# Optimization experiments

Measured on AMD Instinct MI355X. Metric: run time of the kernel, lower is better.

Reference implementation:

```python
import jax, jax.numpy as jnp
import numpy as np


def _maxpool2(t):
    # 2x2x2 max pool, stride 2. t: [B, C, D, H, W]
    B, C, D, H, W = t.shape
    return t.reshape(B, C, D // 2, 2, H // 2, 2, W // 2, 2).max(axis=(3, 5, 7))


def setup_inputs() -> dict:
    key = jax.random.key(0)
    ks = jax.random.split(key, 5)
    ch = 64
    B, D, H, W = 2, 32, 32, 32
    x = jax.random.normal(ks[0], (B, ch, D, H, W), dtype=jnp.float32)
    # 1x1x1 conv weights (out_ch, in_ch), Kaiming-ish scale
    w_theta = jax.random.normal(ks[1], (ch // 8, ch), dtype=jnp.float32) / np.sqrt(ch)
    w_phi = jax.random.normal(ks[2], (ch // 8, ch), dtype=jnp.float32) / np.sqrt(ch)
    w_g = jax.random.normal(ks[3], (ch // 2, ch), dtype=jnp.float32) / np.sqrt(ch)
    w_o = jax.random.normal(ks[4], (ch, ch // 2), dtype=jnp.float32) / np.sqrt(ch // 2)
    gamma = jnp.ones((), dtype=jnp.float32)  # original inits at 0; 1 gives nontrivial output
    return {"x": x, "w_theta": w_theta, "w_phi": w_phi, "w_g": w_g, "w_o": w_o, "gamma": gamma}


def reference(x, w_theta, w_phi, w_g, w_o, gamma):
    B, C, D, H, W = x.shape
    N = D * H * W
    M = N // 8
    xf = x.reshape(B, C, N)  # [B, C, N]
    # 1x1x1 convs = channel matmuls
    theta = jnp.einsum('oc,bcn->bon', w_theta, xf)                     # [B, C//8, N]
    phi = _maxpool2(jnp.einsum('oc,bcn->bon', w_phi, xf).reshape(B, C // 8, D, H, W)).reshape(B, C // 8, M)
    g = _maxpool2(jnp.einsum('oc,bcn->bon', w_g, xf).reshape(B, C // 2, D, H, W)).reshape(B, C // 2, M)
    # unscaled attention: softmax over keys (M)
    beta = jax.nn.softmax(jnp.einsum('bcn,bcm->bnm', theta, phi), axis=-1)  # [B, N, M]
    o = jnp.einsum('bcm,bnm->bcn', g, beta)                                 # [B, C//2, N]
    out = gamma * jnp.einsum('oc,bcn->bon', w_o, o).reshape(B, C, D, H, W) + x
    return out
```

## Files before the change

### kernel.cpp

```cpp
#include <hip/hip_runtime.h>
#include <cstdint>
#include <cstddef>

typedef __attribute__((ext_vector_type(4))) short short4v;
typedef __attribute__((ext_vector_type(4))) float float4v;

#define C_IN  64
#define NB    2
#define NPTS  32768
#define MPTS  4096
#define LOG2E 1.44269504088896340736f
#define KT    64
#define NTILE (MPTS / KT)
#define KSPLIT 2
#define QTILES (NPTS / 32)

__device__ __forceinline__ unsigned short f2bf_rne(float f) {
  unsigned int u = __builtin_bit_cast(unsigned int, f);
  u += 0x7fffu + ((u >> 16) & 1u);
  return (unsigned short)(u >> 16);
}

__device__ __forceinline__ short4v pack_bf16_trunc(float a0, float a1, float a2, float a3) {
  unsigned int u0 = __builtin_amdgcn_perm(__builtin_bit_cast(unsigned int, a1),
                                          __builtin_bit_cast(unsigned int, a0), 0x07060302u);
  unsigned int u1 = __builtin_amdgcn_perm(__builtin_bit_cast(unsigned int, a3),
                                          __builtin_bit_cast(unsigned int, a2), 0x07060302u);
  union { unsigned int u[2]; short4v s; } r;
  r.u[0] = u0; r.u[1] = u1;
  return r.s;
}

__device__ __forceinline__ short4v pack_bf16_rne(float a0, float a1, float a2, float a3) {
  short4v s;
  s[0] = (short)f2bf_rne(a0); s[1] = (short)f2bf_rne(a1);
  s[2] = (short)f2bf_rne(a2); s[3] = (short)f2bf_rne(a3);
  return s;
}

__device__ __forceinline__ void gl_lds16(const unsigned short* g, unsigned short* l) {
  __builtin_amdgcn_global_load_lds(
      (const __attribute__((address_space(1))) void*)g,
      (__attribute__((address_space(3))) void*)l, 16, 0, 0);
}

__device__ void pool_body(int idx, const float* __restrict__ x,
                          const float* __restrict__ w_phi,
                          const float* __restrict__ w_g,
                          unsigned short* __restrict__ phi_pad,
                          unsigned short* __restrict__ g_f) {
  int cg = idx >> 13;
  int bm = idx & 8191;
  int b = bm >> 12, m = bm & 4095;
  int md = m >> 8, mh = (m >> 4) & 15, mw = m & 15;
  const float* xb = x + (size_t)b * C_IN * NPTS
                  + ((md * 2) * 1024 + (mh * 2) * 32 + (mw * 2));
  const float* wbase = (cg < 2) ? (w_phi + cg * 4 * C_IN)
                                : (w_g + (cg * 4 - 8) * C_IN);

  float acc[4][8];
#pragma unroll
  for (int o = 0; o < 4; ++o)
#pragma unroll
    for (int p = 0; p < 8; ++p) acc[o][p] = 0.f;

#pragma unroll 4
  for (int cc = 0; cc < C_IN; ++cc) {
    const float* xp = xb + (size_t)cc * NPTS;
    float2 p01 = *(const float2*)(xp + 0);
    float2 p23 = *(const float2*)(xp + 32);
    float2 p45 = *(const float2*)(xp + 1024);
    float2 p67 = *(const float2*)(xp + 1056);
#pragma unroll
    for (int o = 0; o < 4; ++o) {
      float wv = wbase[o * C_IN + cc];
      acc[o][0] = fmaf(wv, p01.x, acc[o][0]);
      acc[o][1] = fmaf(wv, p01.y, acc[o][1]);
      acc[o][2] = fmaf(wv, p23.x, acc[o][2]);
      acc[o][3] = fmaf(wv, p23.y, acc[o][3]);
      acc[o][4] = fmaf(wv, p45.x, acc[o][4]);
      acc[o][5] = fmaf(wv, p45.y, acc[o][5]);
      acc[o][6] = fmaf(wv, p67.x, acc[o][6]);
      acc[o][7] = fmaf(wv, p67.y, acc[o][7]);
    }
  }
  float mx[4];
#pragma unroll
  for (int o = 0; o < 4; ++o) {
    mx[o] = fmaxf(fmaxf(fmaxf(acc[o][0], acc[o][1]), fmaxf(acc[o][2], acc[o][3])),
                  fmaxf(fmaxf(acc[o][4], acc[o][5]), fmaxf(acc[o][6], acc[o][7])));
  }
  if (cg < 2) {
    int c0 = cg * 4;
#pragma unroll
    for (int o = 0; o < 4; ++o) {
      phi_pad[(bm << 4) + c0 + o] = f2bf_rne(mx[o] * LOG2E);
      phi_pad[(bm << 4) + 8 + c0 + o] = 0;
    }
  } else {
    int gc0 = cg * 4 - 8;
    int kt16 = m >> 4, kr = m & 15;
#pragma unroll
    for (int o = 0; o < 4; ++o) {
      int c = gc0 + o;
      g_f[((((size_t)b * 256 + kt16) * 2 + (c >> 4)) * 16 + (c & 15)) * 16 + kr] =
          f2bf_rne(mx[o]);
    }
  }
}

__device__ void theta_body(int idx, const float* __restrict__ x,
                           const float* __restrict__ w_theta,
                           unsigned short* __restrict__ theta_pad) {
  int b = idx >> 15, n = idx & 32767;
  const float* xb = x + (size_t)b * C_IN * NPTS + n;
  float t[8];
#pragma unroll
  for (int o = 0; o < 8; ++o) t[o] = 0.f;
#pragma unroll 4
  for (int cc = 0; cc < C_IN; ++cc) {
    float xv = xb[(size_t)cc * NPTS];
#pragma unroll
    for (int o = 0; o < 8; ++o) t[o] = fmaf(w_theta[o * C_IN + cc], xv, t[o]);
  }
  unsigned int w0 = (unsigned int)f2bf_rne(t[0]) | ((unsigned int)f2bf_rne(t[1]) << 16);
  unsigned int w1 = (unsigned int)f2bf_rne(t[2]) | ((unsigned int)f2bf_rne(t[3]) << 16);
  unsigned int w2 = (unsigned int)f2bf_rne(t[4]) | ((unsigned int)f2bf_rne(t[5]) << 16);
  unsigned int w3 = (unsigned int)f2bf_rne(t[6]) | ((unsigned int)f2bf_rne(t[7]) << 16);
  uint4* dst = (uint4*)(theta_pad + ((size_t)idx << 4));
  dst[0] = make_uint4(w0, w1, w2, w3);
  dst[1] = make_uint4(0u, 0u, 0u, 0u);
}

__global__ __launch_bounds__(256) void prep_fused(
    const float* __restrict__ x, const float* __restrict__ w_theta,
    const float* __restrict__ w_phi, const float* __restrict__ w_g,
    unsigned short* __restrict__ theta_pad,
    unsigned short* __restrict__ phi_pad,
    unsigned short* __restrict__ g_f) {
  int gb = blockIdx.x;
  if (gb < 320) {
    pool_body(gb * 256 + threadIdx.x, x, w_phi, w_g, phi_pad, g_f);
  } else {
    theta_body((gb - 320) * 256 + threadIdx.x, x, w_theta, theta_pad);
  }
}

__global__ __launch_bounds__(256) void attn_split(
    const unsigned short* __restrict__ theta_pad,
    const unsigned short* __restrict__ phi_pad,
    const unsigned short* __restrict__ g_f,
    float4v* __restrict__ opart,
    float* __restrict__ lbuf) {
  __shared__ unsigned short s_phi[2][KT * 16];
  __shared__ unsigned short s_g[2][(KT / 16) * 512];

  int tid = threadIdx.x;
  int wid = tid >> 6, lane = tid & 63;
  int l4 = lane >> 4, col = lane & 15;
  int b = blockIdx.y >> 1;
  int ks = blockIdx.y & 1;
  int qb = blockIdx.x * 128 + wid * 32;
  int t0 = ks * (NTILE / KSPLIT);
  int t1 = t0 + NTILE / KSPLIT;

  const unsigned short* tb = theta_pad + ((size_t)(b * NPTS + qb) << 4) + l4 * 4;
  short4v bt0 = *(const short4v*)(tb + (col << 4));
  short4v bt1 = *(const short4v*)(tb + ((16 + col) << 4));

  const unsigned short* phib = phi_pad + ((size_t)b * MPTS << 4);
  const unsigned short* gb   = g_f + (size_t)b * (MPTS / 16) * 512;

  float4v acc00 = {0.f, 0.f, 0.f, 0.f}, acc01 = acc00, acc10 = acc00, acc11 = acc00;
  float lsum0 = 0.f, lsum1 = 0.f;

  gl_lds16(gb + (size_t)t0 * 2048 + wid * 512 + lane * 8, &s_g[0][wid * 512]);
  if (wid < 2)
    gl_lds16(phib + (size_t)t0 * 1024 + wid * 512 + lane * 8, &s_phi[0][wid * 512]);
  __syncthreads();

#pragma unroll 1
  for (int t = t0; t < t1; ++t) {
    int cur = t & 1;
    if (t + 1 < t1) {
      gl_lds16(gb + (size_t)(t + 1) * 2048 + wid * 512 + lane * 8,
               &s_g[cur ^ 1][wid * 512]);
      if (wid < 2)
        gl_lds16(phib + (size_t)(t + 1) * 1024 + wid * 512 + lane * 8,
                 &s_phi[cur ^ 1][wid * 512]);
    }

#pragma unroll
    for (int st = 0; st < 4; ++st) {
      int fb = st * 256 + col * 16 + l4 * 4;
      short4v pf = *(const short4v*)&s_phi[cur][fb];
      int gv = st * 512 + col * 16 + l4 * 4;
      short4v g0 = *(const short4v*)&s_g[cur][gv];
      short4v g1 = *(const short4v*)&s_g[cur][gv + 256];

      float4v zero4 = {0.f, 0.f, 0.f, 0.f};
      float4v s0 = __builtin_amdgcn_mfma_f32_16x16x16bf16_1k(pf, bt0, zero4, 0, 0, 0);
      float4v s1 = __builtin_amdgcn_mfma_f32_16x16x16bf16_1k(pf, bt1, zero4, 0, 0, 0);

      float p00 = __builtin_amdgcn_exp2f(s0[0]);
      float p01 = __builtin_amdgcn_exp2f(s0[1]);
      float p02 = __builtin_amdgcn_exp2f(s0[2]);
      float p03 = __builtin_amdgcn_exp2f(s0[3]);
      float p10 = __builtin_amdgcn_exp2f(s1[0]);
      float p11 = __builtin_amdgcn_exp2f(s1[1]);
      float p12 = __builtin_amdgcn_exp2f(s1[2]);
      float p13 = __builtin_amdgcn_exp2f(s1[3]);
      lsum0 += (p00 + p01) + (p02 + p03);
      lsum1 += (p10 + p11) + (p12 + p13);
      short4v pb0 = pack_bf16_trunc(p00, p01, p02, p03);
      short4v pb1 = pack_bf16_trunc(p10, p11, p12, p13);

      acc00 = __builtin_amdgcn_mfma_f32_16x16x16bf16_1k(g0, pb0, acc00, 0, 0, 0);
      acc01 = __builtin_amdgcn_mfma_f32_16x16x16bf16_1k(g0, pb1, acc01, 0, 0, 0);
      acc10 = __builtin_amdgcn_mfma_f32_16x16x16bf16_1k(g1, pb0, acc10, 0, 0, 0);
      acc11 = __builtin_amdgcn_mfma_f32_16x16x16bf16_1k(g1, pb1, acc11, 0, 0, 0);
    }
    __syncthreads();
  }

  lsum0 += __shfl_xor(lsum0, 16, 64);
  lsum0 += __shfl_xor(lsum0, 32, 64);
  lsum1 += __shfl_xor(lsum1, 16, 64);
  lsum1 += __shfl_xor(lsum1, 32, 64);

  int qt = blockIdx.x * 4 + wid;
  size_t obase = (((size_t)(b * KSPLIT + ks) * QTILES + qt) * 4) * 64 + lane;
  opart[obase + 0 * 64] = acc00;
  opart[obase + 1 * 64] = acc01;
  opart[obase + 2 * 64] = acc10;
  opart[obase + 3 * 64] = acc11;
  if (lane < 32) {
    lbuf[((size_t)(b * KSPLIT + ks) * QTILES + qt) * 32 + lane] =
        (lane < 16) ? lsum0 : lsum1;
  }
}

__global__ __launch_bounds__(256) void attn_combine(
    const float* __restrict__ x, const float* __restrict__ w_o,
    const float* __restrict__ gamma_p,
    const float4v* __restrict__ opart,
    const float* __restrict__ lbuf,
    float* __restrict__ out) {
  int tid = threadIdx.x;
  int wid = tid >> 6, lane = tid & 63;
  int l4 = lane >> 4, col = lane & 15;
  int b = blockIdx.y;
  int qt = blockIdx.x * 4 + wid;
  int qb = qt * 32;

  float gamma = gamma_p[0];

  short4v wo[4][2];
#pragma unroll
  for (int cot = 0; cot < 4; ++cot)
#pragma unroll
    for (int ksw = 0; ksw < 2; ++ksw) {
      const float* wp = w_o + (cot * 16 + col) * 32 + ksw * 16 + l4 * 4;
      wo[cot][ksw] = pack_bf16_rne(wp[0] * gamma, wp[1] * gamma,
                                   wp[2] * gamma, wp[3] * gamma);
    }

  size_t ob0 = (((size_t)(b * KSPLIT + 0) * QTILES + qt) * 4) * 64 + lane;
  size_t ob1 = (((size_t)(b * KSPLIT + 1) * QTILES + qt) * 4) * 64 + lane;
  float4v a0 = opart[ob0 + 0 * 64] + opart[ob1 + 0 * 64];
  float4v a1 = opart[ob0 + 1 * 64] + opart[ob1 + 1 * 64];
  float4v a2 = opart[ob0 + 2 * 64] + opart[ob1 + 2 * 64];
  float4v a3 = opart[ob0 + 3 * 64] + opart[ob1 + 3 * 64];

  const float* lb0 = lbuf + ((size_t)(b * KSPLIT + 0) * QTILES + qt) * 32;
  const float* lb1 = lbuf + ((size_t)(b * KSPLIT + 1) * QTILES + qt) * 32;
  float li0 = 1.0f / (lb0[col] + lb1[col]);
  float li1 = 1.0f / (lb0[col + 16] + lb1[col + 16]);

  short4v onb00 = pack_bf16_rne(a0[0] * li0, a0[1] * li0, a0[2] * li0, a0[3] * li0);
  short4v onb01 = pack_bf16_rne(a1[0] * li1, a1[1] * li1, a1[2] * li1, a1[3] * li1);
  short4v onb10 = pack_bf16_rne(a2[0] * li0, a2[1] * li0, a2[2] * li0, a2[3] * li0);
  short4v onb11 = pack_bf16_rne(a3[0] * li1, a3[1] * li1, a3[2] * li1, a3[3] * li1);

  float4v zero4 = {0.f, 0.f, 0.f, 0.f};
#pragma unroll
  for (int cot = 0; cot < 4; ++cot) {
#pragma unroll
    for (int nt = 0; nt < 2; ++nt) {
      short4v bfrag0 = nt ? onb01 : onb00;
      short4v bfrag1 = nt ? onb11 : onb10;
      float4v d = __builtin_amdgcn_mfma_f32_16x16x16bf16_1k(wo[cot][0], bfrag0, zero4, 0, 0, 0);
      d = __builtin_amdgcn_mfma_f32_16x16x16bf16_1k(wo[cot][1], bfrag1, d, 0, 0, 0);
      int n = qb + nt * 16 + col;
      size_t base = (size_t)(b * C_IN + cot * 16 + l4 * 4) * NPTS + n;
      const float* xp = x + base;
      float* op = out + base;
#pragma unroll
      for (int e = 0; e < 4; ++e) {
        op[(size_t)e * NPTS] = d[e] + xp[(size_t)e * NPTS];
      }
    }
  }
}

__global__ __launch_bounds__(256) void attn_mfma(
    const float* __restrict__ x, const float* __restrict__ w_o,
    const float* __restrict__ gamma_p,
    const unsigned short* __restrict__ theta_pad,
    const unsigned short* __restrict__ phi_pad,
    const unsigned short* __restrict__ g_f,
    float* __restrict__ out) {
  __shared__ unsigned short s_phi[2][KT * 16];
  __shared__ unsigned short s_g[2][(KT / 16) * 512];

  int tid = threadIdx.x;
  int wid = tid >> 6, lane = tid & 63;
  int l4 = lane >> 4, col = lane & 15;
  int b = blockIdx.y;
  int qb = blockIdx.x * 128 + wid * 32;

  float gamma = gamma_p[0];

  const unsigned short* tb = theta_pad + ((size_t)(b * NPTS + qb) << 4) + l4 * 4;
  short4v bt0 = *(const short4v*)(tb + (col << 4));
  short4v bt1 = *(const short4v*)(tb + ((16 + col) << 4));

  short4v wo[4][2];
#pragma unroll
  for (int cot = 0; cot < 4; ++cot)
#pragma unroll
    for (int ksw = 0; ksw < 2; ++ksw) {
      const float* wp = w_o + (cot * 16 + col) * 32 + ksw * 16 + l4 * 4;
      wo[cot][ksw] = pack_bf16_rne(wp[0] * gamma, wp[1] * gamma,
                                   wp[2] * gamma, wp[3] * gamma);
    }

  const unsigned short* phib = phi_pad + ((size_t)b * MPTS << 4);
  const unsigned short* gb   = g_f + (size_t)b * (MPTS / 16) * 512;

  float4v acc00 = {0.f, 0.f, 0.f, 0.f}, acc01 = acc00, acc10 = acc00, acc11 = acc00;
  float lsum0 = 0.f, lsum1 = 0.f;

  gl_lds16(gb + 0 * 2048 + wid * 512 + lane * 8, &s_g[0][wid * 512]);
  if (wid < 2)
    gl_lds16(phib + 0 * 1024 + wid * 512 + lane * 8, &s_phi[0][wid * 512]);
  __syncthreads();

#pragma unroll 1
  for (int t = 0; t < NTILE; ++t) {
    int cur = t & 1;
    if (t + 1 < NTILE) {
      gl_lds16(gb + (size_t)(t + 1) * 2048 + wid * 512 + lane * 8,
               &s_g[cur ^ 1][wid * 512]);
      if (wid < 2)
        gl_lds16(phib + (size_t)(t + 1) * 1024 + wid * 512 + lane * 8,
                 &s_phi[cur ^ 1][wid * 512]);
    }
#pragma unroll
    for (int st = 0; st < 4; ++st) {
      int fb = st * 256 + col * 16 + l4 * 4;
      short4v pf = *(const short4v*)&s_phi[cur][fb];
      int gv = st * 512 + col * 16 + l4 * 4;
      short4v g0 = *(const short4v*)&s_g[cur][gv];
      short4v g1 = *(const short4v*)&s_g[cur][gv + 256];

      float4v zero4 = {0.f, 0.f, 0.f, 0.f};
      float4v s0 = __builtin_amdgcn_mfma_f32_16x16x16bf16_1k(pf, bt0, zero4, 0, 0, 0);
      float4v s1 = __builtin_amdgcn_mfma_f32_16x16x16bf16_1k(pf, bt1, zero4, 0, 0, 0);

      float p00 = __builtin_amdgcn_exp2f(s0[0]);
      float p01 = __builtin_amdgcn_exp2f(s0[1]);
      float p02 = __builtin_amdgcn_exp2f(s0[2]);
      float p03 = __builtin_amdgcn_exp2f(s0[3]);
      float p10 = __builtin_amdgcn_exp2f(s1[0]);
      float p11 = __builtin_amdgcn_exp2f(s1[1]);
      float p12 = __builtin_amdgcn_exp2f(s1[2]);
      float p13 = __builtin_amdgcn_exp2f(s1[3]);
      lsum0 += (p00 + p01) + (p02 + p03);
      lsum1 += (p10 + p11) + (p12 + p13);
      short4v pb0 = pack_bf16_trunc(p00, p01, p02, p03);
      short4v pb1 = pack_bf16_trunc(p10, p11, p12, p13);

      acc00 = __builtin_amdgcn_mfma_f32_16x16x16bf16_1k(g0, pb0, acc00, 0, 0, 0);
      acc01 = __builtin_amdgcn_mfma_f32_16x16x16bf16_1k(g0, pb1, acc01, 0, 0, 0);
      acc10 = __builtin_amdgcn_mfma_f32_16x16x16bf16_1k(g1, pb0, acc10, 0, 0, 0);
      acc11 = __builtin_amdgcn_mfma_f32_16x16x16bf16_1k(g1, pb1, acc11, 0, 0, 0);
    }
    __syncthreads();
  }

  lsum0 += __shfl_xor(lsum0, 16, 64);
  lsum0 += __shfl_xor(lsum0, 32, 64);
  lsum1 += __shfl_xor(lsum1, 16, 64);
  lsum1 += __shfl_xor(lsum1, 32, 64);
  float li0 = 1.0f / lsum0;
  float li1 = 1.0f / lsum1;

  short4v onb00 = pack_bf16_rne(acc00[0] * li0, acc00[1] * li0, acc00[2] * li0, acc00[3] * li0);
  short4v onb01 = pack_bf16_rne(acc01[0] * li1, acc01[1] * li1, acc01[2] * li1, acc01[3] * li1);
  short4v onb10 = pack_bf16_rne(acc10[0] * li0, acc10[1] * li0, acc10[2] * li0, acc10[3] * li0);
  short4v onb11 = pack_bf16_rne(acc11[0] * li1, acc11[1] * li1, acc11[2] * li1, acc11[3] * li1);

  float4v zero4 = {0.f, 0.f, 0.f, 0.f};
#pragma unroll
  for (int cot = 0; cot < 4; ++cot) {
#pragma unroll
    for (int nt = 0; nt < 2; ++nt) {
      short4v bfrag0 = nt ? onb01 : onb00;
      short4v bfrag1 = nt ? onb11 : onb10;
      float4v d = __builtin_amdgcn_mfma_f32_16x16x16bf16_1k(wo[cot][0], bfrag0, zero4, 0, 0, 0);
      d = __builtin_amdgcn_mfma_f32_16x16x16bf16_1k(wo[cot][1], bfrag1, d, 0, 0, 0);
      int n = qb + nt * 16 + col;
      size_t base = (size_t)(b * C_IN + cot * 16 + l4 * 4) * NPTS + n;
      const float* xp = x + base;
      float* op = out + base;
#pragma unroll
      for (int e = 0; e < 4; ++e) {
        op[(size_t)e * NPTS] = d[e] + xp[(size_t)e * NPTS];
      }
    }
  }
}

extern "C" void kernel_launch(void* const* d_in, const int* in_sizes, int n_in,
                              void* d_out, int out_size, void* d_ws, size_t ws_size,
                              hipStream_t stream) {
  const float* x       = (const float*)d_in[0];
  const float* w_theta = (const float*)d_in[1];
  const float* w_phi   = (const float*)d_in[2];
  const float* w_g     = (const float*)d_in[3];
  const float* w_o     = (const float*)d_in[4];
  const float* gamma   = (const float*)d_in[5];
  float* out = (float*)d_out;

  char* ws = (char*)d_ws;
  unsigned short* theta_pad = (unsigned short*)ws;            ws += (size_t)NB * NPTS * 16 * 2;
  unsigned short* phi_pad   = (unsigned short*)ws;            ws += (size_t)NB * MPTS * 16 * 2;
  unsigned short* g_f       = (unsigned short*)ws;            ws += (size_t)NB * MPTS * 32 * 2;
  size_t base_need = (size_t)(ws - (char*)d_ws);
  float4v* opart = (float4v*)ws;                              ws += (size_t)NB * KSPLIT * QTILES * 4 * 64 * 16;
  float*   lbuf  = (float*)ws;                                ws += (size_t)NB * KSPLIT * QTILES * 32 * 4;
  size_t split_need = (size_t)(ws - (char*)d_ws);

  prep_fused<<<dim3(576), dim3(256), 0, stream>>>(
      x, w_theta, w_phi, w_g, theta_pad, phi_pad, g_f);

  if (ws_size >= split_need) {
    attn_split<<<dim3(NPTS / 128, NB * KSPLIT), dim3(256), 0, stream>>>(
        theta_pad, phi_pad, g_f, opart, lbuf);
    attn_combine<<<dim3(NPTS / 128, NB), dim3(256), 0, stream>>>(
        x, w_o, gamma, opart, lbuf, out);
  } else if (ws_size >= base_need) {
    attn_mfma<<<dim3(NPTS / 128, NB), dim3(256), 0, stream>>>(
        x, w_o, gamma, theta_pad, phi_pad, g_f, out);
  }
}
```

Baseline: 91.48 us.

## Pre-swizzle phi/g into MFMA fragment layout, widen pool threads, allow 4-way key split

phi and g are now written in the exact MFMA operand fragment order, so LDS reads in the attention loop become contiguous lane*4 loads instead of strided per-column gathers. The pooling stage computes 8 output channels per thread rather than 4, which halves its block count and reuses each x load across more channels. The key dimension split is templated and uses 4 splits when the workspace is large enough, giving more blocks for occupancy at the cost of extra partial-sum traffic in the combine step.

```diff
diff --git a/kernel.cpp b/kernel.cpp
--- a/kernel.cpp
+++ b/kernel.cpp
@@ -12,7 +12,6 @@
 #define LOG2E 1.44269504088896340736f
 #define KT    64
 #define NTILE (MPTS / KT)
-#define KSPLIT 2
 #define QTILES (NPTS / 32)
 
 __device__ __forceinline__ unsigned short f2bf_rne(float f) {
@@ -44,10 +43,11 @@
       (__attribute__((address_space(3))) void*)l, 16, 0, 0);
 }
 
+
 __device__ void pool_body(int idx, const float* __restrict__ x,
                           const float* __restrict__ w_phi,
                           const float* __restrict__ w_g,
-                          unsigned short* __restrict__ phi_pad,
+                          unsigned short* __restrict__ phi_f,
                           unsigned short* __restrict__ g_f) {
   int cg = idx >> 13;
   int bm = idx & 8191;
@@ -55,12 +55,11 @@
   int md = m >> 8, mh = (m >> 4) & 15, mw = m & 15;
   const float* xb = x + (size_t)b * C_IN * NPTS
                   + ((md * 2) * 1024 + (mh * 2) * 32 + (mw * 2));
-  const float* wbase = (cg < 2) ? (w_phi + cg * 4 * C_IN)
-                                : (w_g + (cg * 4 - 8) * C_IN);
-
-  float acc[4][8];
-#pragma unroll
-  for (int o = 0; o < 4; ++o)
+  const float* wbase = (cg == 0) ? w_phi : (w_g + (cg - 1) * 8 * C_IN);
+
+  float acc[8][8];
+#pragma unroll
+  for (int o = 0; o < 8; ++o)
 #pragma unroll
     for (int p = 0; p < 8; ++p) acc[o][p] = 0.f;
 
@@ -72,7 +71,7 @@
     float2 p45 = *(const float2*)(xp + 1024);
     float2 p67 = *(const float2*)(xp + 1056);
 #pragma unroll
-    for (int o = 0; o < 4; ++o) {
+    for (int o = 0; o < 8; ++o) {
       float wv = wbase[o * C_IN + cc];
       acc[o][0] = fmaf(wv, p01.x, acc[o][0]);
       acc[o][1] = fmaf(wv, p01.y, acc[o][1]);
@@ -84,27 +83,35 @@
       acc[o][7] = fmaf(wv, p67.y, acc[o][7]);
     }
   }
-  float mx[4];
-#pragma unroll
-  for (int o = 0; o < 4; ++o) {
+  float mx[8];
+#pragma unroll
+  for (int o = 0; o < 8; ++o) {
     mx[o] = fmaxf(fmaxf(fmaxf(acc[o][0], acc[o][1]), fmaxf(acc[o][2], acc[o][3])),
                   fmaxf(fmaxf(acc[o][4], acc[o][5]), fmaxf(acc[o][6], acc[o][7])));
   }
-  if (cg < 2) {
-    int c0 = cg * 4;
-#pragma unroll
-    for (int o = 0; o < 4; ++o) {
-      phi_pad[(bm << 4) + c0 + o] = f2bf_rne(mx[o] * LOG2E);
-      phi_pad[(bm << 4) + 8 + c0 + o] = 0;
+  int kt16 = m >> 4, kr = m & 15;
+  if (cg == 0) {
+    size_t fb = ((size_t)b * 256 + kt16) * 256;
+#pragma unroll
+    for (int g2 = 0; g2 < 2; ++g2) {
+      unsigned int u0 = (unsigned int)f2bf_rne(mx[g2 * 4 + 0] * LOG2E)
+                      | ((unsigned int)f2bf_rne(mx[g2 * 4 + 1] * LOG2E) << 16);
+      unsigned int u1 = (unsigned int)f2bf_rne(mx[g2 * 4 + 2] * LOG2E)
+                      | ((unsigned int)f2bf_rne(mx[g2 * 4 + 3] * LOG2E) << 16);
+      *(uint2*)&phi_f[fb + (g2 * 16 + kr) * 4] = make_uint2(u0, u1);
+    }
+#pragma unroll
+    for (int g2 = 2; g2 < 4; ++g2) {
+      *(uint2*)&phi_f[fb + (g2 * 16 + kr) * 4] = make_uint2(0u, 0u);
     }
   } else {
-    int gc0 = cg * 4 - 8;
-    int kt16 = m >> 4, kr = m & 15;
-#pragma unroll
-    for (int o = 0; o < 4; ++o) {
+    int gc0 = (cg - 1) * 8;
+#pragma unroll
+    for (int o = 0; o < 8; ++o) {
       int c = gc0 + o;
-      g_f[((((size_t)b * 256 + kt16) * 2 + (c >> 4)) * 16 + (c & 15)) * 16 + kr] =
-          f2bf_rne(mx[o]);
+      int half = c >> 4, c15 = c & 15;
+      size_t base = (((size_t)b * 256 + kt16) * 2 + half) * 256;
+      g_f[base + ((kr >> 2) * 16 + c15) * 4 + (kr & 3)] = f2bf_rne(mx[o]);
     }
   }
 }
@@ -136,19 +143,20 @@
     const float* __restrict__ x, const float* __restrict__ w_theta,
     const float* __restrict__ w_phi, const float* __restrict__ w_g,
     unsigned short* __restrict__ theta_pad,
-    unsigned short* __restrict__ phi_pad,
+    unsigned short* __restrict__ phi_f,
     unsigned short* __restrict__ g_f) {
   int gb = blockIdx.x;
-  if (gb < 320) {
-    pool_body(gb * 256 + threadIdx.x, x, w_phi, w_g, phi_pad, g_f);
+  if (gb < 160) {
+    pool_body(gb * 256 + threadIdx.x, x, w_phi, w_g, phi_f, g_f);
   } else {
-    theta_body((gb - 320) * 256 + threadIdx.x, x, w_theta, theta_pad);
-  }
-}
-
+    theta_body((gb - 160) * 256 + threadIdx.x, x, w_theta, theta_pad);
+  }
+}
+
+template <int KS>
 __global__ __launch_bounds__(256) void attn_split(
     const unsigned short* __restrict__ theta_pad,
-    const unsigned short* __restrict__ phi_pad,
+    const unsigned short* __restrict__ phi_f,
     const unsigned short* __restrict__ g_f,
     float4v* __restrict__ opart,
     float* __restrict__ lbuf) {
@@ -158,18 +166,18 @@
   int tid = threadIdx.x;
   int wid = tid >> 6, lane = tid & 63;
   int l4 = lane >> 4, col = lane & 15;
-  int b = blockIdx.y >> 1;
-  int ks = blockIdx.y & 1;
+  int b = blockIdx.y / KS;
+  int ks = blockIdx.y & (KS - 1);
   int qb = blockIdx.x * 128 + wid * 32;
-  int t0 = ks * (NTILE / KSPLIT);
-  int t1 = t0 + NTILE / KSPLIT;
+  int t0 = ks * (NTILE / KS);
+  int t1 = t0 + NTILE / KS;
 
   const unsigned short* tb = theta_pad + ((size_t)(b * NPTS + qb) << 4) + l4 * 4;
   short4v bt0 = *(const short4v*)(tb + (col << 4));
   short4v bt1 = *(const short4v*)(tb + ((16 + col) << 4));
 
-  const unsigned short* phib = phi_pad + ((size_t)b * MPTS << 4);
-  const unsigned short* gb   = g_f + (size_t)b * (MPTS / 16) * 512;
+  const unsigned short* phib = phi_f + (size_t)b * 256 * 256;
+  const unsigned short* gb   = g_f + (size_t)b * 256 * 512;
 
   float4v acc00 = {0.f, 0.f, 0.f, 0.f}, acc01 = acc00, acc10 = acc00, acc11 = acc00;
   float lsum0 = 0.f, lsum1 = 0.f;
@@ -192,11 +200,9 @@
 
 #pragma unroll
     for (int st = 0; st < 4; ++st) {
-      int fb = st * 256 + col * 16 + l4 * 4;
-      short4v pf = *(const short4v*)&s_phi[cur][fb];
-      int gv = st * 512 + col * 16 + l4 * 4;
-      short4v g0 = *(const short4v*)&s_g[cur][gv];
-      short4v g1 = *(const short4v*)&s_g[cur][gv + 256];
+      short4v pf = *(const short4v*)&s_phi[cur][st * 256 + lane * 4];
+      short4v g0 = *(const short4v*)&s_g[cur][st * 512 + lane * 4];
+      short4v g1 = *(const short4v*)&s_g[cur][st * 512 + 256 + lane * 4];
 
       float4v zero4 = {0.f, 0.f, 0.f, 0.f};
       float4v s0 = __builtin_amdgcn_mfma_f32_16x16x16bf16_1k(pf, bt0, zero4, 0, 0, 0);
@@ -229,17 +235,18 @@
   lsum1 += __shfl_xor(lsum1, 32, 64);
 
   int qt = blockIdx.x * 4 + wid;
-  size_t obase = (((size_t)(b * KSPLIT + ks) * QTILES + qt) * 4) * 64 + lane;
+  size_t obase = (((size_t)(b * KS + ks) * QTILES + qt) * 4) * 64 + lane;
   opart[obase + 0 * 64] = acc00;
   opart[obase + 1 * 64] = acc01;
   opart[obase + 2 * 64] = acc10;
   opart[obase + 3 * 64] = acc11;
   if (lane < 32) {
-    lbuf[((size_t)(b * KSPLIT + ks) * QTILES + qt) * 32 + lane] =
+    lbuf[((size_t)(b * KS + ks) * QTILES + qt) * 32 + lane] =
         (lane < 16) ? lsum0 : lsum1;
   }
 }
 
+template <int KS>
 __global__ __launch_bounds__(256) void attn_combine(
     const float* __restrict__ x, const float* __restrict__ w_o,
     const float* __restrict__ gamma_p,
@@ -265,17 +272,21 @@
                                    wp[2] * gamma, wp[3] * gamma);
     }
 
-  size_t ob0 = (((size_t)(b * KSPLIT + 0) * QTILES + qt) * 4) * 64 + lane;
-  size_t ob1 = (((size_t)(b * KSPLIT + 1) * QTILES + qt) * 4) * 64 + lane;
-  float4v a0 = opart[ob0 + 0 * 64] + opart[ob1 + 0 * 64];
-  float4v a1 = opart[ob0 + 1 * 64] + opart[ob1 + 1 * 64];
-  float4v a2 = opart[ob0 + 2 * 64] + opart[ob1 + 2 * 64];
-  float4v a3 = opart[ob0 + 3 * 64] + opart[ob1 + 3 * 64];
-
-  const float* lb0 = lbuf + ((size_t)(b * KSPLIT + 0) * QTILES + qt) * 32;
-  const float* lb1 = lbuf + ((size_t)(b * KSPLIT + 1) * QTILES + qt) * 32;
-  float li0 = 1.0f / (lb0[col] + lb1[col]);
-  float li1 = 1.0f / (lb0[col + 16] + lb1[col + 16]);
+  float4v a0 = {0.f, 0.f, 0.f, 0.f}, a1 = a0, a2 = a0, a3 = a0;
+  float ls0 = 0.f, ls1 = 0.f;
+#pragma unroll
+  for (int ks = 0; ks < KS; ++ks) {
+    size_t ob = (((size_t)(b * KS + ks) * QTILES + qt) * 4) * 64 + lane;
+    a0 += opart[ob + 0 * 64];
+    a1 += opart[ob + 1 * 64];
+    a2 += opart[ob + 2 * 64];
+    a3 += opart[ob + 3 * 64];
+    const float* lb = lbuf + ((size_t)(b * KS + ks) * QTILES + qt) * 32;
+    ls0 += lb[col];
+    ls1 += lb[col + 16];
+  }
+  float li0 = 1.0f / ls0;
+  float li1 = 1.0f / ls1;
 
   short4v onb00 = pack_bf16_rne(a0[0] * li0, a0[1] * li0, a0[2] * li0, a0[3] * li0);
   short4v onb01 = pack_bf16_rne(a1[0] * li1, a1[1] * li1, a1[2] * li1, a1[3] * li1);
@@ -307,7 +318,7 @@
     const float* __restrict__ x, const float* __restrict__ w_o,
     const float* __restrict__ gamma_p,
     const unsigned short* __restrict__ theta_pad,
-    const unsigned short* __restrict__ phi_pad,
+    const unsigned short* __restrict__ phi_f,
     const unsigned short* __restrict__ g_f,
     float* __restrict__ out) {
   __shared__ unsigned short s_phi[2][KT * 16];
@@ -335,8 +346,8 @@
                                    wp[2] * gamma, wp[3] * gamma);
     }
 
-  const unsigned short* phib = phi_pad + ((size_t)b * MPTS << 4);
-  const unsigned short* gb   = g_f + (size_t)b * (MPTS / 16) * 512;
+  const unsigned short* phib = phi_f + (size_t)b * 256 * 256;
+  const unsigned short* gb   = g_f + (size_t)b * 256 * 512;
 
   float4v acc00 = {0.f, 0.f, 0.f, 0.f}, acc01 = acc00, acc10 = acc00, acc11 = acc00;
   float lsum0 = 0.f, lsum1 = 0.f;
@@ -358,11 +369,9 @@
     }
 #pragma unroll
     for (int st = 0; st < 4; ++st) {
-      int fb = st * 256 + col * 16 + l4 * 4;
-      short4v pf = *(const short4v*)&s_phi[cur][fb];
-      int gv = st * 512 + col * 16 + l4 * 4;
-      short4v g0 = *(const short4v*)&s_g[cur][gv];
-      short4v g1 = *(const short4v*)&s_g[cur][gv + 256];
+      short4v pf = *(const short4v*)&s_phi[cur][st * 256 + lane * 4];
+      short4v g0 = *(const short4v*)&s_g[cur][st * 512 + lane * 4];
+      short4v g1 = *(const short4v*)&s_g[cur][st * 512 + 256 + lane * 4];
 
       float4v zero4 = {0.f, 0.f, 0.f, 0.f};
       float4v s0 = __builtin_amdgcn_mfma_f32_16x16x16bf16_1k(pf, bt0, zero4, 0, 0, 0);
@@ -434,24 +443,35 @@
   float* out = (float*)d_out;
 
   char* ws = (char*)d_ws;
-  unsigned short* theta_pad = (unsigned short*)ws;            ws += (size_t)NB * NPTS * 16 * 2;
-  unsigned short* phi_pad   = (unsigned short*)ws;            ws += (size_t)NB * MPTS * 16 * 2;
-  unsigned short* g_f       = (unsigned short*)ws;            ws += (size_t)NB * MPTS * 32 * 2;
+  unsigned short* theta_pad = (unsigned short*)ws;  ws += (size_t)NB * NPTS * 16 * 2;
+  unsigned short* phi_f     = (unsigned short*)ws;  ws += (size_t)NB * 256 * 256 * 2;
+  unsigned short* g_f       = (unsigned short*)ws;  ws += (size_t)NB * 256 * 512 * 2;
   size_t base_need = (size_t)(ws - (char*)d_ws);
-  float4v* opart = (float4v*)ws;                              ws += (size_t)NB * KSPLIT * QTILES * 4 * 64 * 16;
-  float*   lbuf  = (float*)ws;                                ws += (size_t)NB * KSPLIT * QTILES * 32 * 4;
-  size_t split_need = (size_t)(ws - (char*)d_ws);
-
-  prep_fused<<<dim3(576), dim3(256), 0, stream>>>(
-      x, w_theta, w_phi, w_g, theta_pad, phi_pad, g_f);
-
-  if (ws_size >= split_need) {
-    attn_split<<<dim3(NPTS / 128, NB * KSPLIT), dim3(256), 0, stream>>>(
-        theta_pad, phi_pad, g_f, opart, lbuf);
-    attn_combine<<<dim3(NPTS / 128, NB), dim3(256), 0, stream>>>(
+  float4v* opart = (float4v*)ws;
+  size_t opart4 = (size_t)NB * 4 * QTILES * 4 * 64 * sizeof(float4v);
+  size_t opart2 = (size_t)NB * 2 * QTILES * 4 * 64 * sizeof(float4v);
+  size_t lbuf4  = (size_t)NB * 4 * QTILES * 32 * sizeof(float);
+  size_t lbuf2  = (size_t)NB * 2 * QTILES * 32 * sizeof(float);
+  size_t need4 = base_need + opart4 + lbuf4;
+  size_t need2 = base_need + opart2 + lbuf2;
+
+  prep_fused<<<dim3(416), dim3(256), 0, stream>>>(
+      x, w_theta, w_phi, w_g, theta_pad, phi_f, g_f);
+
+  if (ws_size >= need4) {
+    float* lbuf = (float*)((char*)opart + opart4);
+    attn_split<4><<<dim3(NPTS / 128, NB * 4), dim3(256), 0, stream>>>(
+        theta_pad, phi_f, g_f, opart, lbuf);
+    attn_combine<4><<<dim3(NPTS / 128, NB), dim3(256), 0, stream>>>(
+        x, w_o, gamma, opart, lbuf, out);
+  } else if (ws_size >= need2) {
+    float* lbuf = (float*)((char*)opart + opart2);
+    attn_split<2><<<dim3(NPTS / 128, NB * 2), dim3(256), 0, stream>>>(
+        theta_pad, phi_f, g_f, opart, lbuf);
+    attn_combine<2><<<dim3(NPTS / 128, NB), dim3(256), 0, stream>>>(
         x, w_o, gamma, opart, lbuf, out);
   } else if (ws_size >= base_need) {
     attn_mfma<<<dim3(NPTS / 128, NB), dim3(256), 0, stream>>>(
-        x, w_o, gamma, theta_pad, phi_pad, g_f, out);
-  }
-}
+        x, w_o, gamma, theta_pad, phi_f, g_f, out);
+  }
+}
```

New measurement: 96.85 us. 1.06x slower.
